# Optimization experiments

Hardware: AMD Instinct MI355X
Metric: run time of the kernel (lower is better)

The kernel has to match this reference:

```python
import jax, jax.numpy as jnp
import numpy as np

N_NODES = 100000
N_EDGES = 1600000
N_GRAPHS = 256
IN_DIM, HID, OUT_DIM = 20, 128, 30954


def setup_inputs() -> dict:
    key = jax.random.key(0)
    ks = jax.random.split(key, 9)
    x = jax.random.normal(ks[0], (N_NODES, IN_DIM), dtype=jnp.float32)
    edge_index = jax.random.randint(ks[1], (2, N_EDGES), 0, N_NODES, dtype=jnp.int64)
    batch = jnp.sort(jax.random.randint(ks[2], (N_NODES,), 0, N_GRAPHS, dtype=jnp.int64))
    s = 0.05
    W1 = jax.random.normal(ks[3], (IN_DIM, HID), dtype=jnp.float32) * s
    b1 = jax.random.normal(ks[4], (HID,), dtype=jnp.float32) * s
    W2 = jax.random.normal(ks[5], (HID, HID), dtype=jnp.float32) * s
    b2 = jax.random.normal(ks[6], (HID,), dtype=jnp.float32) * s
    Wc = jax.random.normal(ks[7], (HID, OUT_DIM), dtype=jnp.float32) * s
    bc = jax.random.normal(ks[8], (OUT_DIM,), dtype=jnp.float32) * s
    return {"x": x, "edge_index": edge_index, "batch": batch,
            "W1": W1, "b1": b1, "W2": W2, "b2": b2, "Wc": Wc, "bc": bc}


def _gcn_norm(edge_index, n_nodes):
    # add self loops (PyG GCNConv default), symmetric normalization
    loops = jnp.arange(n_nodes, dtype=edge_index.dtype)
    src = jnp.concatenate([edge_index[0], loops])
    dst = jnp.concatenate([edge_index[1], loops])
    deg = jax.ops.segment_sum(jnp.ones_like(dst, dtype=jnp.float32), dst,
                              num_segments=n_nodes)
    dinv = jnp.where(deg > 0, jax.lax.rsqrt(deg), 0.0)
    norm = dinv[src] * dinv[dst]  # [E+N]
    return src, dst, norm


def _gcn_conv(x, src, dst, norm, W, b, n_nodes):
    h = x @ W                              # [N, out] transform first (fewer msg flops)
    msg = h[src] * norm[:, None]           # gather + scale
    out = jax.ops.segment_sum(msg, dst, num_segments=n_nodes)
    return out + b


def reference(x, edge_index, batch, W1, b1, W2, b2, Wc, bc):
    n = x.shape[0]
    src, dst, norm = _gcn_norm(edge_index, n)
    h = jax.nn.relu(_gcn_conv(x, src, dst, norm, W1, b1, n))
    # dropout is identity in eval mode
    h = jax.nn.relu(_gcn_conv(h, src, dst, norm, W2, b2, n))
    # global mean pool per graph
    sums = jax.ops.segment_sum(h, batch, num_segments=N_GRAPHS)       # [G, HID]
    cnts = jax.ops.segment_sum(jnp.ones((n,), jnp.float32), batch,
                               num_segments=N_GRAPHS)
    pooled = sums / jnp.maximum(cnts, 1.0)[:, None]
    return pooled @ Wc + bc  # [G, OUT_DIM]
```

## Files before the change

### kernel.cpp

```cpp
#include <hip/hip_runtime.h>

#define HID 128
#define SCAN_B 256

__device__ __forceinline__ float bf_lo(unsigned int u) { return __uint_as_float(u << 16); }
__device__ __forceinline__ float bf_hi(unsigned int u) { return __uint_as_float(u & 0xFFFF0000u); }
__device__ __forceinline__ unsigned short f2bf(float f) {
    unsigned int u = __float_as_uint(f);
    unsigned int r = (u + 0x7FFFu + ((u >> 16) & 1u)) >> 16;
    return (unsigned short)r;
}

__global__ void detect_kernel(const unsigned int* __restrict__ p, int* __restrict__ flag) {
    if (threadIdx.x == 0 && blockIdx.x == 0) {
        int is64 = 1;
        for (int i = 0; i < 64; ++i) {
            if (p[2 * i + 1] != 0u) { is64 = 0; break; }
        }
        *flag = is64;
    }
}

__global__ void cvtdeg_kernel(const void* __restrict__ p, int* __restrict__ out,
                              int* __restrict__ deg, int E, const int* __restrict__ flag) {
    int i = blockIdx.x * blockDim.x + threadIdx.x;
    if (i < 2 * E) {
        int v = (*flag) ? (int)((const long long*)p)[i] : ((const int*)p)[i];
        out[i] = v;
        if (i >= E) atomicAdd(&deg[v], 1);
    }
}

__global__ void zero_kernel(float4* __restrict__ p, long long n4) {
    long long i = (long long)blockIdx.x * blockDim.x + threadIdx.x;
    long long stride = (long long)gridDim.x * blockDim.x;
    for (; i < n4; i += stride) p[i] = make_float4(0.f, 0.f, 0.f, 0.f);
}

__global__ void cvtx_kernel(const float* __restrict__ x, unsigned short* __restrict__ xb, int n) {
    int i = blockIdx.x * blockDim.x + threadIdx.x;
    if (i < n) xb[i] = f2bf(x[i]);
}

__global__ __launch_bounds__(SCAN_B) void scan1_kernel(const int* __restrict__ deg,
                                                       int* __restrict__ incl,
                                                       int* __restrict__ blockSums, int N) {
    __shared__ int s[SCAN_B];
    int i = blockIdx.x * SCAN_B + threadIdx.x;
    int v = (i < N) ? deg[i] : 0;
    s[threadIdx.x] = v;
    __syncthreads();
#pragma unroll
    for (int off = 1; off < SCAN_B; off <<= 1) {
        int t = (threadIdx.x >= off) ? s[threadIdx.x - off] : 0;
        __syncthreads();
        s[threadIdx.x] += t;
        __syncthreads();
    }
    if (i < N) incl[i] = s[threadIdx.x];
    if (threadIdx.x == SCAN_B - 1) blockSums[blockIdx.x] = s[SCAN_B - 1];
}

__global__ __launch_bounds__(1024) void scan2_kernel(int* __restrict__ blockSums, int nb) {
    __shared__ int s[1024];
    int v = (threadIdx.x < nb) ? blockSums[threadIdx.x] : 0;
    s[threadIdx.x] = v;
    __syncthreads();
#pragma unroll
    for (int off = 1; off < 1024; off <<= 1) {
        int t = (threadIdx.x >= off) ? s[threadIdx.x - off] : 0;
        __syncthreads();
        s[threadIdx.x] += t;
        __syncthreads();
    }
    if (threadIdx.x < nb) blockSums[threadIdx.x] = (threadIdx.x > 0) ? s[threadIdx.x - 1] : 0;
}

__global__ void scan3_kernel(const int* __restrict__ incl, const int* __restrict__ deg,
                             const int* __restrict__ blockSums, int* __restrict__ rowstart,
                             float* __restrict__ dinv, int* __restrict__ cursor,
                             int N, int E) {
    int i = blockIdx.x * blockDim.x + threadIdx.x;
    if (i < N) {
        int d = deg[i];
        rowstart[i] = incl[i] - d + blockSums[i / SCAN_B];
        dinv[i] = rsqrtf((float)(d + 1));
        cursor[i] = 0;
    }
    if (i == 0) rowstart[N] = E;
}

__global__ void scatter_kernel(const int* __restrict__ src, const int* __restrict__ dst,
                               const int* __restrict__ rowstart, int* __restrict__ cursor,
                               int2* __restrict__ elist, const float* __restrict__ dinv, int E) {
    int e = blockIdx.x * blockDim.x + threadIdx.x;
    if (e >= E) return;
    int s = src[e], d = dst[e];
    int pos = rowstart[d] + atomicAdd(&cursor[d], 1);
    float nm = dinv[s] * dinv[d];
    elist[pos] = make_int2(s, __float_as_int(nm));
}

__global__ void gstart_kernel(const void* __restrict__ bt, const int* __restrict__ flag,
                              int* __restrict__ gstart, int N, int G) {
    int g = blockIdx.x * blockDim.x + threadIdx.x;
    if (g > G) return;
    int is64 = *flag;
    int lo = 0, hi = N;
    while (lo < hi) {
        int mid = (lo + hi) >> 1;
        int v = is64 ? (int)((const long long*)bt)[mid] : ((const int*)bt)[mid];
        if (v < g) lo = mid + 1; else hi = mid;
    }
    gstart[g] = lo;
}

__global__ __launch_bounds__(256) void agg_lin1_kernel(const float* __restrict__ x,
                                                       const unsigned int* __restrict__ xb32,
                                                       const float* __restrict__ W,
                                                       const float* __restrict__ b,
                                                       float* __restrict__ h,
                                                       const int* __restrict__ rowstart,
                                                       const int2* __restrict__ elist,
                                                       const float* __restrict__ dinv,
                                                       int N, int IN) {
    __shared__ float Ws[20 * HID];
    __shared__ float zs[8][20];
    const int tid = threadIdx.x;
    for (int i = tid; i < IN * HID; i += 256) Ws[i] = W[i];

    const int g      = tid >> 5;
    const int lane32 = tid & 31;
    const int slot   = lane32 >> 4;
    const int l      = lane32 & 15;
    const int node   = blockIdx.x * 8 + g;
    const int half   = IN >> 1;
    const bool act   = (node < N) && (l < half);

    float accx = 0.f, accy = 0.f;
    if (node < N) {
        int beg = rowstart[node], end = rowstart[node + 1];
        int e = beg + slot;
        for (; e + 2 < end; e += 4) {
            int2 p0 = elist[e];
            int2 p1 = elist[e + 2];
            unsigned int u0 = act ? xb32[(size_t)p0.x * half + l] : 0u;
            unsigned int u1 = act ? xb32[(size_t)p1.x * half + l] : 0u;
            float n0 = __int_as_float(p0.y), n1 = __int_as_float(p1.y);
            accx += bf_lo(u0) * n0 + bf_lo(u1) * n1;
            accy += bf_hi(u0) * n0 + bf_hi(u1) * n1;
        }
        if (e < end) {
            int2 p0 = elist[e];
            unsigned int u0 = act ? xb32[(size_t)p0.x * half + l] : 0u;
            float n0 = __int_as_float(p0.y);
            accx += bf_lo(u0) * n0;
            accy += bf_hi(u0) * n0;
        }
    }
    accx += __shfl_xor(accx, 16, 64);
    accy += __shfl_xor(accy, 16, 64);
    if (node < N && slot == 0 && l < half) {
        float di = dinv[node];
        float dd = di * di;
        zs[g][2 * l]     = accx + x[(size_t)node * IN + 2 * l] * dd;
        zs[g][2 * l + 1] = accy + x[(size_t)node * IN + 2 * l + 1] * dd;
    }
    __syncthreads();

    if (node < N) {
        const int j = lane32;
        float4 acc4 = ((const float4*)b)[j];
        for (int k = 0; k < IN; ++k) {
            float zv = zs[g][k];
            float4 w = *(const float4*)&Ws[k * HID + j * 4];
            acc4.x += zv * w.x; acc4.y += zv * w.y;
            acc4.z += zv * w.z; acc4.w += zv * w.w;
        }
        acc4.x = fmaxf(acc4.x, 0.f); acc4.y = fmaxf(acc4.y, 0.f);
        acc4.z = fmaxf(acc4.z, 0.f); acc4.w = fmaxf(acc4.w, 0.f);
        ((float4*)h)[(size_t)node * 32 + j] = acc4;
    }
}

#define TBM 64
#define TBN 64
#define TBK 32
#define XLD (TBM + 4)

__global__ __launch_bounds__(256) void gemm128_kernel(const float* __restrict__ A,
                                                      const float* __restrict__ W,
                                                      unsigned short* __restrict__ Cb, int N) {
    __shared__ float xs[TBK][XLD];
    __shared__ float wsh[TBK][TBN + 4];
    const int tid = threadIdx.x;
    const int n0 = blockIdx.x * TBM;
    const int c0 = blockIdx.y * TBN;
    const int ng = tid >> 4;
    const int cg = tid & 15;
    const int anode = tid >> 3;
    const int af    = tid & 7;
    const int wk    = tid >> 4;
    const int wc    = tid & 15;

    float acc[4][4] = {};

    for (int k0 = 0; k0 < HID; k0 += TBK) {
#pragma unroll
        for (int r = 0; r < 2; ++r) {
            int node = anode + r * 32;
            int gn = n0 + node;
            float4 v = make_float4(0.f, 0.f, 0.f, 0.f);
            if (gn < N) v = *(const float4*)(A + (size_t)gn * HID + k0 + af * 4);
            xs[af * 4 + 0][node] = v.x;
            xs[af * 4 + 1][node] = v.y;
            xs[af * 4 + 2][node] = v.z;
            xs[af * 4 + 3][node] = v.w;
        }
#pragma unroll
        for (int r = 0; r < 2; ++r) {
            int kk = wk + r * 16;
            *(float4*)&wsh[kk][wc * 4] =
                *(const float4*)(W + (size_t)(k0 + kk) * HID + c0 + wc * 4);
        }
        __syncthreads();
#pragma unroll
        for (int kk = 0; kk < TBK; ++kk) {
            float a[4], b[4];
            *(float4*)a = *(const float4*)&xs[kk][ng * 4];
            *(float4*)b = *(const float4*)&wsh[kk][cg * 4];
#pragma unroll
            for (int m = 0; m < 4; ++m)
#pragma unroll
                for (int n = 0; n < 4; ++n) acc[m][n] += a[m] * b[n];
        }
        __syncthreads();
    }

#pragma unroll
    for (int m = 0; m < 4; ++m) {
        int gn = n0 + ng * 4 + m;
        if (gn < N) {
            ushort4 st;
            st.x = f2bf(acc[m][0]); st.y = f2bf(acc[m][1]);
            st.z = f2bf(acc[m][2]); st.w = f2bf(acc[m][3]);
            *(ushort4*)(Cb + (size_t)gn * HID + c0 + cg * 4) = st;
        }
    }
}

__global__ __launch_bounds__(256) void csr_aggb_kernel(const unsigned short* __restrict__ h2b,
                                                       unsigned short* __restrict__ outb,
                                                       const int* __restrict__ rowstart,
                                                       const int2* __restrict__ elist,
                                                       const float* __restrict__ dinv,
                                                       const float* __restrict__ bias,
                                                       int N) {
    int node = blockIdx.x * 16 + (threadIdx.x >> 4);
    if (node >= N) return;
    int q = threadIdx.x & 15;
    const uint4* hv = (const uint4*)h2b;
    float acc[8] = {};
    int beg = rowstart[node], end = rowstart[node + 1];
    int e = beg;
    for (; e + 3 < end; e += 4) {
        int2 p0 = elist[e];
        int2 p1 = elist[e + 1];
        int2 p2 = elist[e + 2];
        int2 p3 = elist[e + 3];
        uint4 a0 = hv[(size_t)p0.x * 16 + q];
        uint4 a1 = hv[(size_t)p1.x * 16 + q];
        uint4 a2 = hv[(size_t)p2.x * 16 + q];
        uint4 a3 = hv[(size_t)p3.x * 16 + q];
        float n0 = __int_as_float(p0.y), n1 = __int_as_float(p1.y);
        float n2 = __int_as_float(p2.y), n3 = __int_as_float(p3.y);
        acc[0] += bf_lo(a0.x) * n0 + bf_lo(a1.x) * n1 + bf_lo(a2.x) * n2 + bf_lo(a3.x) * n3;
        acc[1] += bf_hi(a0.x) * n0 + bf_hi(a1.x) * n1 + bf_hi(a2.x) * n2 + bf_hi(a3.x) * n3;
        acc[2] += bf_lo(a0.y) * n0 + bf_lo(a1.y) * n1 + bf_lo(a2.y) * n2 + bf_lo(a3.y) * n3;
        acc[3] += bf_hi(a0.y) * n0 + bf_hi(a1.y) * n1 + bf_hi(a2.y) * n2 + bf_hi(a3.y) * n3;
        acc[4] += bf_lo(a0.z) * n0 + bf_lo(a1.z) * n1 + bf_lo(a2.z) * n2 + bf_lo(a3.z) * n3;
        acc[5] += bf_hi(a0.z) * n0 + bf_hi(a1.z) * n1 + bf_hi(a2.z) * n2 + bf_hi(a3.z) * n3;
        acc[6] += bf_lo(a0.w) * n0 + bf_lo(a1.w) * n1 + bf_lo(a2.w) * n2 + bf_lo(a3.w) * n3;
        acc[7] += bf_hi(a0.w) * n0 + bf_hi(a1.w) * n1 + bf_hi(a2.w) * n2 + bf_hi(a3.w) * n3;
    }
    for (; e < end; ++e) {
        int2 p0 = elist[e];
        uint4 a0 = hv[(size_t)p0.x * 16 + q];
        float n0 = __int_as_float(p0.y);
        acc[0] += bf_lo(a0.x) * n0; acc[1] += bf_hi(a0.x) * n0;
        acc[2] += bf_lo(a0.y) * n0; acc[3] += bf_hi(a0.y) * n0;
        acc[4] += bf_lo(a0.z) * n0; acc[5] += bf_hi(a0.z) * n0;
        acc[6] += bf_lo(a0.w) * n0; acc[7] += bf_hi(a0.w) * n0;
    }
    float di = dinv[node];
    float dd = di * di;
    uint4 sv = hv[(size_t)node * 16 + q];
    float self[8] = { bf_lo(sv.x), bf_hi(sv.x), bf_lo(sv.y), bf_hi(sv.y),
                      bf_lo(sv.z), bf_hi(sv.z), bf_lo(sv.w), bf_hi(sv.w) };
    float4 b0 = ((const float4*)bias)[2 * q];
    float4 b1 = ((const float4*)bias)[2 * q + 1];
    float r[8];
    r[0] = fmaxf(acc[0] + self[0] * dd + b0.x, 0.f);
    r[1] = fmaxf(acc[1] + self[1] * dd + b0.y, 0.f);
    r[2] = fmaxf(acc[2] + self[2] * dd + b0.z, 0.f);
    r[3] = fmaxf(acc[3] + self[3] * dd + b0.w, 0.f);
    r[4] = fmaxf(acc[4] + self[4] * dd + b1.x, 0.f);
    r[5] = fmaxf(acc[5] + self[5] * dd + b1.y, 0.f);
    r[6] = fmaxf(acc[6] + self[6] * dd + b1.z, 0.f);
    r[7] = fmaxf(acc[7] + self[7] * dd + b1.w, 0.f);
    uint4 st;
    st.x = (unsigned)f2bf(r[0]) | ((unsigned)f2bf(r[1]) << 16);
    st.y = (unsigned)f2bf(r[2]) | ((unsigned)f2bf(r[3]) << 16);
    st.z = (unsigned)f2bf(r[4]) | ((unsigned)f2bf(r[5]) << 16);
    st.w = (unsigned)f2bf(r[6]) | ((unsigned)f2bf(r[7]) << 16);
    ((uint4*)outb)[(size_t)node * 16 + q] = st;
}

__global__ __launch_bounds__(1024) void pool2_kernel(const unsigned short* __restrict__ hb,
                                                     const int* __restrict__ gstart,
                                                     float* __restrict__ meanp, int G) {
    int g = blockIdx.x;
    int part = threadIdx.x >> 7;
    int j = threadIdx.x & 127;
    int beg = gstart[g], end = gstart[g + 1];
    float s = 0.f;
    for (int n = beg + part; n < end; n += 8)
        s += __uint_as_float(((unsigned)hb[(size_t)n * HID + j]) << 16);
    __shared__ float red[8][HID];
    red[part][j] = s;
    __syncthreads();
    if (part == 0) {
        float tot = 0.f;
#pragma unroll
        for (int r = 0; r < 8; ++r) tot += red[r][j];
        float c = (float)(end - beg);
        meanp[(size_t)g * HID + j] = tot / fmaxf(c, 1.f);
    }
}

#define CBM 64
#define CBN 64
#define CBK 32

__global__ __launch_bounds__(256) void clsgemm_kernel(const float* __restrict__ A,
                                                      const float* __restrict__ Bw,
                                                      const float* __restrict__ bc,
                                                      float* __restrict__ C,
                                                      int G, int OUT) {
    __shared__ float as[CBK][CBM + 4];
    __shared__ float bs[CBK][CBN + 4];
    const int tid = threadIdx.x;
    const int g0 = blockIdx.y * CBM;
    const int c0 = blockIdx.x * CBN;
    const int mg = tid >> 4;
    const int cg = tid & 15;
    const int arow = tid >> 3;
    const int af   = tid & 7;
    const int wk   = tid >> 4;
    const int wc   = tid & 15;

    float acc[4][4] = {};

    for (int k0 = 0; k0 < HID; k0 += CBK) {
#pragma unroll
        for (int r = 0; r < 2; ++r) {
            int row = arow + r * 32;
            int g = g0 + row;
            float4 v = make_float4(0.f, 0.f, 0.f, 0.f);
            if (g < G) v = *(const float4*)(A + (size_t)g * HID + k0 + af * 4);
            as[af * 4 + 0][row] = v.x;
            as[af * 4 + 1][row] = v.y;
            as[af * 4 + 2][row] = v.z;
            as[af * 4 + 3][row] = v.w;
        }
#pragma unroll
        for (int r = 0; r < 2; ++r) {
            int kk = wk + r * 16;
            int c = c0 + wc * 4;
            const float* bp = Bw + (size_t)(k0 + kk) * OUT + c;
            float2 lo = make_float2(0.f, 0.f), hi = make_float2(0.f, 0.f);
            if (c + 3 < OUT) {
                lo = *(const float2*)bp;
                hi = *(const float2*)(bp + 2);
            } else {
                if (c + 0 < OUT) lo.x = bp[0];
                if (c + 1 < OUT) lo.y = bp[1];
                if (c + 2 < OUT) hi.x = bp[2];
                if (c + 3 < OUT) hi.y = bp[3];
            }
            bs[kk][wc * 4 + 0] = lo.x;
            bs[kk][wc * 4 + 1] = lo.y;
            bs[kk][wc * 4 + 2] = hi.x;
            bs[kk][wc * 4 + 3] = hi.y;
        }
        __syncthreads();
#pragma unroll
        for (int kk = 0; kk < CBK; ++kk) {
            float a[4], b[4];
            *(float4*)a = *(const float4*)&as[kk][mg * 4];
            *(float4*)b = *(const float4*)&bs[kk][cg * 4];
#pragma unroll
            for (int m = 0; m < 4; ++m)
#pragma unroll
                for (int n = 0; n < 4; ++n) acc[m][n] += a[m] * b[n];
        }
        __syncthreads();
    }

    int c = c0 + cg * 4;
    float b0 = (c + 0 < OUT) ? bc[c + 0] : 0.f;
    float b1 = (c + 1 < OUT) ? bc[c + 1] : 0.f;
    float b2 = (c + 2 < OUT) ? bc[c + 2] : 0.f;
    float b3 = (c + 3 < OUT) ? bc[c + 3] : 0.f;
#pragma unroll
    for (int m = 0; m < 4; ++m) {
        int g = g0 + mg * 4 + m;
        if (g >= G) continue;
        float* cp = C + (size_t)g * OUT + c;
        if (c + 3 < OUT) {
            *(float2*)cp = make_float2(acc[m][0] + b0, acc[m][1] + b1);
            *(float2*)(cp + 2) = make_float2(acc[m][2] + b2, acc[m][3] + b3);
        } else {
            if (c + 0 < OUT) cp[0] = acc[m][0] + b0;
            if (c + 1 < OUT) cp[1] = acc[m][1] + b1;
            if (c + 2 < OUT) cp[2] = acc[m][2] + b2;
            if (c + 3 < OUT) cp[3] = acc[m][3] + b3;
        }
    }
}

extern "C" void kernel_launch(void* const* d_in, const int* in_sizes, int n_in,
                              void* d_out, int out_size, void* d_ws, size_t ws_size,
                              hipStream_t stream) {
    const float* x  = (const float*)d_in[0];
    const void*  ei = d_in[1];
    const void*  bt = d_in[2];
    const float* W1 = (const float*)d_in[3];
    const float* b1 = (const float*)d_in[4];
    const float* W2 = (const float*)d_in[5];
    const float* b2 = (const float*)d_in[6];
    const float* Wc = (const float*)d_in[7];
    const float* bc = (const float*)d_in[8];
    float* out = (float*)d_out;

    const int N   = in_sizes[2];
    const int E   = in_sizes[1] / 2;
    const int IN  = in_sizes[0] / N;
    const int OUT = in_sizes[8];
    const int G   = out_size / OUT;

    char* ws = (char*)d_ws;
    size_t off = 0;
    auto alloc = [&](size_t bytes) {
        size_t p = off;
        off += (bytes + 255) & ~(size_t)255;
        return p;
    };
    int*            idx32    = (int*)(ws + alloc((size_t)2 * E * 4));
    int*            deg      = (int*)(ws + alloc((size_t)N * 4));
    float*          dinv     = (float*)(ws + alloc((size_t)N * 4));
    int*            incl     = (int*)(ws + alloc((size_t)N * 4));
    int*            rowstart = (int*)(ws + alloc((size_t)(N + 1) * 4));
    int*            cursor   = (int*)(ws + alloc((size_t)N * 4));
    int*            blockSums= (int*)(ws + alloc((size_t)1024 * 4));
    int2*           elist    = (int2*)(ws + alloc((size_t)E * 8));
    unsigned short* xb       = (unsigned short*)(ws + alloc((size_t)N * IN * 2));
    float*          bufA     = (float*)(ws + alloc((size_t)N * HID * 4));
    unsigned short* h2b      = (unsigned short*)(ws + alloc((size_t)N * HID * 2));
    int*            gstart   = (int*)(ws + alloc((size_t)(G + 1) * 4));
    float*          meanp    = (float*)(ws + alloc((size_t)G * HID * 4));
    int*            flag     = (int*)(ws + alloc(4));
    (void)ws_size;

    int* srcI = idx32;
    int* dstI = idx32 + E;
    unsigned short* houtb = (unsigned short*)bufA;

    const int B = 256;
    const int nb = (N + SCAN_B - 1) / SCAN_B;

    detect_kernel<<<1, 64, 0, stream>>>((const unsigned int*)ei, flag);
    zero_kernel<<<256, B, 0, stream>>>((float4*)deg, (long long)N / 4);
    cvtdeg_kernel<<<(2 * E + B - 1) / B, B, 0, stream>>>(ei, idx32, deg, E, flag);
    cvtx_kernel<<<(N * IN + B - 1) / B, B, 0, stream>>>(x, xb, N * IN);

    scan1_kernel<<<nb, SCAN_B, 0, stream>>>(deg, incl, blockSums, N);
    scan2_kernel<<<1, 1024, 0, stream>>>(blockSums, nb);
    scan3_kernel<<<(N + B - 1) / B, B, 0, stream>>>(incl, deg, blockSums, rowstart,
                                                    dinv, cursor, N, E);
    scatter_kernel<<<(E + B - 1) / B, B, 0, stream>>>(srcI, dstI, rowstart, cursor, elist, dinv, E);

    gstart_kernel<<<2, 256, 0, stream>>>(bt, flag, gstart, N, G);

    agg_lin1_kernel<<<(N + 7) / 8, 256, 0, stream>>>(x, (const unsigned int*)xb, W1, b1,
                                                     bufA, rowstart, elist, dinv, N, IN);

    {
        dim3 grid((N + TBM - 1) / TBM, HID / TBN);
        gemm128_kernel<<<grid, 256, 0, stream>>>(bufA, W2, h2b, N);
    }
    csr_aggb_kernel<<<(N + 15) / 16, 256, 0, stream>>>(h2b, houtb, rowstart, elist, dinv, b2, N);

    pool2_kernel<<<G, 1024, 0, stream>>>(houtb, gstart, meanp, G);

    {
        dim3 grid((OUT + CBN - 1) / CBN, (G + CBM - 1) / CBM);
        clsgemm_kernel<<<grid, 256, 0, stream>>>(meanp, Wc, bc, out, G, OUT);
    }
}
```

Measured before the change: 385.0 us.

## Store layer-1 activations in bf16, vectorize edge scatter, unroll aggregation loop

The first GCN layer's output now goes to a bf16 buffer, and the 128x128 GEMM reads it as packed bf16 and widens it to fp32 in shared memory. This halves the bytes written and re-read for the intermediate activations. The edge scatter kernel now handles four edges per thread with int4 loads, and the layer-1 gather loop is unrolled to four edges per slot to keep more loads in flight. The trade-off is extra rounding of hidden activations to bf16 before the second transform.

```diff
diff --git a/kernel.cpp b/kernel.cpp
--- a/kernel.cpp
+++ b/kernel.cpp
@@ -93,12 +93,29 @@
 __global__ void scatter_kernel(const int* __restrict__ src, const int* __restrict__ dst,
                                const int* __restrict__ rowstart, int* __restrict__ cursor,
                                int2* __restrict__ elist, const float* __restrict__ dinv, int E) {
-    int e = blockIdx.x * blockDim.x + threadIdx.x;
-    if (e >= E) return;
-    int s = src[e], d = dst[e];
-    int pos = rowstart[d] + atomicAdd(&cursor[d], 1);
-    float nm = dinv[s] * dinv[d];
-    elist[pos] = make_int2(s, __float_as_int(nm));
+    int t = blockIdx.x * blockDim.x + threadIdx.x;
+    int e0 = t * 4;
+    if (e0 + 3 < E) {
+        int4 s4 = *(const int4*)(src + e0);
+        int4 d4 = *(const int4*)(dst + e0);
+        float ds0 = dinv[s4.x], ds1 = dinv[s4.y], ds2 = dinv[s4.z], ds3 = dinv[s4.w];
+        float dd0 = dinv[d4.x], dd1 = dinv[d4.y], dd2 = dinv[d4.z], dd3 = dinv[d4.w];
+        int r0 = rowstart[d4.x], r1 = rowstart[d4.y], r2 = rowstart[d4.z], r3 = rowstart[d4.w];
+        int p0 = r0 + atomicAdd(&cursor[d4.x], 1);
+        int p1 = r1 + atomicAdd(&cursor[d4.y], 1);
+        int p2 = r2 + atomicAdd(&cursor[d4.z], 1);
+        int p3 = r3 + atomicAdd(&cursor[d4.w], 1);
+        elist[p0] = make_int2(s4.x, __float_as_int(ds0 * dd0));
+        elist[p1] = make_int2(s4.y, __float_as_int(ds1 * dd1));
+        elist[p2] = make_int2(s4.z, __float_as_int(ds2 * dd2));
+        elist[p3] = make_int2(s4.w, __float_as_int(ds3 * dd3));
+    } else {
+        for (int e = e0; e < E; ++e) {
+            int s = src[e], d = dst[e];
+            int pos = rowstart[d] + atomicAdd(&cursor[d], 1);
+            elist[pos] = make_int2(s, __float_as_int(dinv[s] * dinv[d]));
+        }
+    }
 }
 
 __global__ void gstart_kernel(const void* __restrict__ bt, const int* __restrict__ flag,
@@ -119,7 +136,7 @@
                                                        const unsigned int* __restrict__ xb32,
                                                        const float* __restrict__ W,
                                                        const float* __restrict__ b,
-                                                       float* __restrict__ h,
+                                                       unsigned int* __restrict__ h1b,
                                                        const int* __restrict__ rowstart,
                                                        const int2* __restrict__ elist,
                                                        const float* __restrict__ dinv,
@@ -141,16 +158,21 @@
     if (node < N) {
         int beg = rowstart[node], end = rowstart[node + 1];
         int e = beg + slot;
-        for (; e + 2 < end; e += 4) {
+        for (; e + 6 < end; e += 8) {
             int2 p0 = elist[e];
             int2 p1 = elist[e + 2];
+            int2 p2 = elist[e + 4];
+            int2 p3 = elist[e + 6];
             unsigned int u0 = act ? xb32[(size_t)p0.x * half + l] : 0u;
             unsigned int u1 = act ? xb32[(size_t)p1.x * half + l] : 0u;
+            unsigned int u2 = act ? xb32[(size_t)p2.x * half + l] : 0u;
+            unsigned int u3 = act ? xb32[(size_t)p3.x * half + l] : 0u;
             float n0 = __int_as_float(p0.y), n1 = __int_as_float(p1.y);
-            accx += bf_lo(u0) * n0 + bf_lo(u1) * n1;
-            accy += bf_hi(u0) * n0 + bf_hi(u1) * n1;
-        }
-        if (e < end) {
+            float n2 = __int_as_float(p2.y), n3 = __int_as_float(p3.y);
+            accx += bf_lo(u0) * n0 + bf_lo(u1) * n1 + bf_lo(u2) * n2 + bf_lo(u3) * n3;
+            accy += bf_hi(u0) * n0 + bf_hi(u1) * n1 + bf_hi(u2) * n2 + bf_hi(u3) * n3;
+        }
+        for (; e < end; e += 2) {
             int2 p0 = elist[e];
             unsigned int u0 = act ? xb32[(size_t)p0.x * half + l] : 0u;
             float n0 = __int_as_float(p0.y);
@@ -179,7 +201,10 @@
         }
         acc4.x = fmaxf(acc4.x, 0.f); acc4.y = fmaxf(acc4.y, 0.f);
         acc4.z = fmaxf(acc4.z, 0.f); acc4.w = fmaxf(acc4.w, 0.f);
-        ((float4*)h)[(size_t)node * 32 + j] = acc4;
+        uint2 st;
+        st.x = (unsigned)f2bf(acc4.x) | ((unsigned)f2bf(acc4.y) << 16);
+        st.y = (unsigned)f2bf(acc4.z) | ((unsigned)f2bf(acc4.w) << 16);
+        ((uint2*)h1b)[(size_t)node * 32 + j] = st;
     }
 }
 
@@ -188,7 +213,7 @@
 #define TBK 32
 #define XLD (TBM + 4)
 
-__global__ __launch_bounds__(256) void gemm128_kernel(const float* __restrict__ A,
+__global__ __launch_bounds__(256) void gemm128_kernel(const unsigned int* __restrict__ Ab,
                                                       const float* __restrict__ W,
                                                       unsigned short* __restrict__ Cb, int N) {
     __shared__ float xs[TBK][XLD];
@@ -198,24 +223,29 @@
     const int c0 = blockIdx.y * TBN;
     const int ng = tid >> 4;
     const int cg = tid & 15;
-    const int anode = tid >> 3;
-    const int af    = tid & 7;
+    const int anode = tid >> 2;
+    const int af    = tid & 3;
     const int wk    = tid >> 4;
     const int wc    = tid & 15;
 
+    const uint4* Av = (const uint4*)Ab;
+
     float acc[4][4] = {};
 
     for (int k0 = 0; k0 < HID; k0 += TBK) {
-#pragma unroll
-        for (int r = 0; r < 2; ++r) {
-            int node = anode + r * 32;
-            int gn = n0 + node;
-            float4 v = make_float4(0.f, 0.f, 0.f, 0.f);
-            if (gn < N) v = *(const float4*)(A + (size_t)gn * HID + k0 + af * 4);
-            xs[af * 4 + 0][node] = v.x;
-            xs[af * 4 + 1][node] = v.y;
-            xs[af * 4 + 2][node] = v.z;
-            xs[af * 4 + 3][node] = v.w;
+        {
+            int gn = n0 + anode;
+            uint4 u = make_uint4(0u, 0u, 0u, 0u);
+            if (gn < N) u = Av[(size_t)gn * 16 + (k0 >> 3) + af];
+            int kb = af * 8;
+            xs[kb + 0][anode] = bf_lo(u.x);
+            xs[kb + 1][anode] = bf_hi(u.x);
+            xs[kb + 2][anode] = bf_lo(u.y);
+            xs[kb + 3][anode] = bf_hi(u.y);
+            xs[kb + 4][anode] = bf_lo(u.z);
+            xs[kb + 5][anode] = bf_hi(u.z);
+            xs[kb + 6][anode] = bf_lo(u.w);
+            xs[kb + 7][anode] = bf_hi(u.w);
         }
 #pragma unroll
         for (int r = 0; r < 2; ++r) {
@@ -465,8 +495,9 @@
     int*            blockSums= (int*)(ws + alloc((size_t)1024 * 4));
     int2*           elist    = (int2*)(ws + alloc((size_t)E * 8));
     unsigned short* xb       = (unsigned short*)(ws + alloc((size_t)N * IN * 2));
-    float*          bufA     = (float*)(ws + alloc((size_t)N * HID * 4));
+    unsigned int*   h1b      = (unsigned int*)(ws + alloc((size_t)N * HID * 2));
     unsigned short* h2b      = (unsigned short*)(ws + alloc((size_t)N * HID * 2));
+    unsigned short* houtb    = (unsigned short*)(ws + alloc((size_t)N * HID * 2));
     int*            gstart   = (int*)(ws + alloc((size_t)(G + 1) * 4));
     float*          meanp    = (float*)(ws + alloc((size_t)G * HID * 4));
     int*            flag     = (int*)(ws + alloc(4));
@@ -474,7 +505,6 @@
 
     int* srcI = idx32;
     int* dstI = idx32 + E;
-    unsigned short* houtb = (unsigned short*)bufA;
 
     const int B = 256;
     const int nb = (N + SCAN_B - 1) / SCAN_B;
@@ -488,16 +518,20 @@
     scan2_kernel<<<1, 1024, 0, stream>>>(blockSums, nb);
     scan3_kernel<<<(N + B - 1) / B, B, 0, stream>>>(incl, deg, blockSums, rowstart,
                                                     dinv, cursor, N, E);
-    scatter_kernel<<<(E + B - 1) / B, B, 0, stream>>>(srcI, dstI, rowstart, cursor, elist, dinv, E);
+    {
+        int nt = (E + 3) / 4;
+        scatter_kernel<<<(nt + B - 1) / B, B, 0, stream>>>(srcI, dstI, rowstart, cursor,
+                                                           elist, dinv, E);
+    }
 
     gstart_kernel<<<2, 256, 0, stream>>>(bt, flag, gstart, N, G);
 
     agg_lin1_kernel<<<(N + 7) / 8, 256, 0, stream>>>(x, (const unsigned int*)xb, W1, b1,
-                                                     bufA, rowstart, elist, dinv, N, IN);
+                                                     h1b, rowstart, elist, dinv, N, IN);
 
     {
         dim3 grid((N + TBM - 1) / TBM, HID / TBN);
-        gemm128_kernel<<<grid, 256, 0, stream>>>(bufA, W2, h2b, N);
+        gemm128_kernel<<<grid, 256, 0, stream>>>(h1b, W2, h2b, N);
     }
     csr_aggb_kernel<<<(N + 15) / 16, 256, 0, stream>>>(h2b, houtb, rowstart, elist, dinv, b2, N);
 
```

Result: slower. 462.0 us (+20.0%).
